# Optimization experiments

Hardware: AMD Instinct MI355X
Metric: run time of the kernel (lower is better)

Reference implementation:

```python
import jax, jax.numpy as jnp
import numpy as np
import math

N, S, D, H, L, F = 4, 2048, 512, 8, 4, 200
HD = D // H
EPS = 1e-5


def _pos_encoding(seq_len, d_model, dtype):
    pos = jnp.arange(seq_len, dtype=jnp.float32)[:, None]            # [S,1]
    div = jnp.exp(jnp.arange(0, d_model, 2, dtype=jnp.float32) * (-math.log(10000.0) / d_model))
    ang = pos * div                                                   # [S,D/2]
    pe = jnp.stack([jnp.sin(ang), jnp.cos(ang)], axis=-1).reshape(seq_len, d_model)
    return pe.astype(dtype)


def _layernorm(x, w, b):
    mu = jnp.mean(x, axis=-1, keepdims=True)
    var = jnp.mean(jnp.square(x - mu), axis=-1, keepdims=True)
    return (x - mu) * jax.lax.rsqrt(var + EPS) * w + b


def setup_inputs() -> dict:
    key = jax.random.key(0)
    ks = jax.random.split(key, 8)
    std = 0.02
    inp = {
        "features": jax.random.normal(ks[0], (N, S, D), dtype=jnp.float32),
        # attention projections, stored as [L, in, out] (math-equivalent to torch x @ W.T + b)
        "Wq": jax.random.normal(ks[1], (L, D, D), dtype=jnp.float32) * std,
        "bq": jnp.zeros((L, D), dtype=jnp.float32),
        "Wk": jax.random.normal(ks[2], (L, D, D), dtype=jnp.float32) * std,
        "bk": jnp.zeros((L, D), dtype=jnp.float32),
        "Wv": jax.random.normal(ks[3], (L, D, D), dtype=jnp.float32) * std,
        "bv": jnp.zeros((L, D), dtype=jnp.float32),
        "Wo": jax.random.normal(ks[4], (L, D, D), dtype=jnp.float32) * std,
        "bo": jnp.zeros((L, D), dtype=jnp.float32),
        # FFN
        "W1": jax.random.normal(ks[5], (L, D, F), dtype=jnp.float32) * std,
        "b1": jnp.zeros((L, F), dtype=jnp.float32),
        "W2": jax.random.normal(ks[6], (L, F, D), dtype=jnp.float32) * std,
        "b2": jnp.zeros((L, D), dtype=jnp.float32),
        # layernorms
        "ln1_w": jnp.ones((L, D), dtype=jnp.float32),
        "ln1_b": jnp.zeros((L, D), dtype=jnp.float32),
        "ln2_w": jnp.ones((L, D), dtype=jnp.float32),
        "ln2_b": jnp.zeros((L, D), dtype=jnp.float32),
    }
    return inp


def _encoder(features, Wq, bq, Wk, bk, Wv, bv, Wo, bo, W1, b1, W2, b2,
             ln1_w, ln1_b, ln2_w, ln2_b):
    n, s, d = features.shape
    x = features + _pos_encoding(s, d, features.dtype)[None]  # PositionalEncoding (dropout=identity in eval)
    scale = 1.0 / math.sqrt(HD)
    for l in range(L):
        # MultiHeadAttention: manual QK^T -> softmax -> AV
        q = (x @ Wq[l] + bq[l]).reshape(n, s, H, HD)
        k = (x @ Wk[l] + bk[l]).reshape(n, s, H, HD)
        v = (x @ Wv[l] + bv[l]).reshape(n, s, H, HD)
        attn = jnp.einsum("nshd,nthd->nhst", q, k) * scale          # [N,H,S,S]
        score = jax.nn.softmax(attn, axis=-1)
        y = jnp.einsum("nhst,nthd->nshd", score, v).reshape(n, s, d)
        attn_out = y @ Wo[l] + bo[l]
        x = _layernorm(x + attn_out, ln1_w[l], ln1_b[l])
        # FFN: linear2(relu(linear1(x)))
        ff = jax.nn.relu(x @ W1[l] + b1[l]) @ W2[l] + b2[l]
        x = _layernorm(x + ff, ln2_w[l], ln2_b[l])
    return x


def reference(features, Wq, bq, Wk, bk, Wv, bv, Wo, bo, W1, b1, W2, b2,
              ln1_w, ln1_b, ln2_w, ln2_b):
    return _encoder(features, Wq, bq, Wk, bk, Wv, bv, Wo, bo, W1, b1, W2, b2,
                    ln1_w, ln1_b, ln2_w, ln2_b)
```

## Files before the change

kernel.cpp:

```cpp
#include <hip/hip_runtime.h>
#include <hip/hip_bf16.h>
#include <cstdint>


typedef __bf16 bf16;
typedef __bf16 bf16x8 __attribute__((ext_vector_type(8)));
typedef __bf16 bf16x4 __attribute__((ext_vector_type(4)));
typedef short short4v __attribute__((ext_vector_type(4)));
typedef float f32x4 __attribute__((ext_vector_type(4)));

#define MFMA16(a, b, c) __builtin_amdgcn_mfma_f32_16x16x32_bf16((a), (b), (c), 0, 0, 0)

__device__ __forceinline__ f32x4 mfma_k16(bf16x4 a, bf16x4 b, f32x4 c) {
#if __has_builtin(__builtin_amdgcn_mfma_f32_16x16x16_bf16)
    return __builtin_amdgcn_mfma_f32_16x16x16_bf16(a, b, c, 0, 0, 0);
#else
    short4v as, bs;
    __builtin_memcpy(&as, &a, 8);
    __builtin_memcpy(&bs, &b, 8);
    return __builtin_amdgcn_mfma_f32_16x16x16bf16_1k(as, bs, c, 0, 0, 0);
#endif
}

static constexpr int NB   = 4;
static constexpr int SQ   = 2048;
static constexpr int DM   = 512;
static constexpr int NH   = 8;
static constexpr int HD   = 64;
static constexpr int NL   = 4;
static constexpr int FF   = 200;
static constexpr int FFP  = 256;
static constexpr int MTOK = NB * SQ;

__device__ __forceinline__ float fast_exp2(float x) {
#if __has_builtin(__builtin_amdgcn_exp2f)
    return __builtin_amdgcn_exp2f(x);
#else
    return exp2f(x);
#endif
}

__device__ __forceinline__ void gld16(bf16* l, const bf16* g) {
    __builtin_amdgcn_global_load_lds(
        (const __attribute__((address_space(1))) void*)g,
        (__attribute__((address_space(3))) void*)l, 16, 0, 0);
}

__global__ __launch_bounds__(256) void convw_kernel(
    const float* __restrict__ Wq, const float* __restrict__ Wk,
    const float* __restrict__ Wv, const float* __restrict__ Wo,
    const float* __restrict__ W1, const float* __restrict__ W2,
    bf16* __restrict__ wqkvt, bf16* __restrict__ wot,
    bf16* __restrict__ w1t, bf16* __restrict__ w2t)
{
    __shared__ float tile[32][33];
    const int z = blockIdx.z, l = z / 6, which = z % 6;
    const float* src; bf16* dst; int K, Nsrc, Npad, Kpad;
    switch (which) {
        case 0: src = Wq + (size_t)l*DM*DM; dst = wqkvt + (size_t)(l*3+0)*DM*DM; K=DM; Nsrc=DM; Npad=DM; Kpad=DM; break;
        case 1: src = Wk + (size_t)l*DM*DM; dst = wqkvt + (size_t)(l*3+1)*DM*DM; K=DM; Nsrc=DM; Npad=DM; Kpad=DM; break;
        case 2: src = Wv + (size_t)l*DM*DM; dst = wqkvt + (size_t)(l*3+2)*DM*DM; K=DM; Nsrc=DM; Npad=DM; Kpad=DM; break;
        case 3: src = Wo + (size_t)l*DM*DM; dst = wot   + (size_t)l*DM*DM;       K=DM; Nsrc=DM; Npad=DM; Kpad=DM; break;
        case 4: src = W1 + (size_t)l*DM*FF; dst = w1t   + (size_t)l*FFP*DM;      K=DM; Nsrc=FF; Npad=FFP; Kpad=DM; break;
        default:src = W2 + (size_t)l*FF*DM; dst = w2t   + (size_t)l*DM*FFP;      K=FF; Nsrc=DM; Npad=DM; Kpad=FFP; break;
    }
    const int k0 = blockIdx.x * 32, n0 = blockIdx.y * 32;
    if (k0 >= Kpad || n0 >= Npad) return;
    const int tr = threadIdx.x >> 3, tc = (threadIdx.x & 7) * 4;
    for (int c = 0; c < 4; c++) {
        int sr = k0 + tr, sc = n0 + tc + c;
        tile[tr][tc + c] = (sr < K && sc < Nsrc) ? src[(size_t)sr * Nsrc + sc] : 0.f;
    }
    __syncthreads();
    const int dr = n0 + tr;
    if (dr < Npad) {
        for (int c = 0; c < 4; c++) {
            int dc = k0 + tc + c;
            if (dc < Kpad) dst[(size_t)dr * Kpad + dc] = (bf16)tile[tc + c][tr];
        }
    }
}

__global__ __launch_bounds__(256) void posenc_kernel(
    const float* __restrict__ f, float* __restrict__ x, bf16* __restrict__ xb)
{
    const int t = blockIdx.x * 256 + threadIdx.x;
    const int d2 = t & 255, row = t >> 8, s = row & (SQ - 1);
    const float kfac = -0.03597789207803197f;
    float dv = __expf((float)d2 * kfac);
    float ang = (float)s * dv;
    float pe0 = sinf(ang), pe1 = cosf(ang);
    const size_t base = (size_t)row * DM + d2 * 2;
    float2 fv = *(const float2*)(f + base);
    float o0 = fv.x + pe0, o1 = fv.y + pe1;
    *(float2*)(x + base) = make_float2(o0, o1);
    union { bf16 h[2]; unsigned int u; } pk;
    pk.h[0] = (bf16)o0; pk.h[1] = (bf16)o1;
    *(unsigned int*)(xb + base) = pk.u;
}

__device__ __forceinline__ void gemm128_core(
    const bf16* __restrict__ A, const bf16* __restrict__ Wt, int K,
    int m0, int n0, bf16* As, bf16* Bs, f32x4 (&acc)[4][4])
{
    const int tid = threadIdx.x;
    const int w = tid >> 6, lane = tid & 63;
    const int l15 = lane & 15, quad = lane >> 4;
    const int srow = w * 16 + (lane >> 2);
    const int scol = (lane & 3) * 8;
    const bf16* Ag = A  + (size_t)(m0 + srow) * K + scol;
    const bf16* Bg = Wt + (size_t)(n0 + srow) * K + scol;
    bf16* AsW = As + w * 512;
    bf16* BsW = Bs + w * 512;
    const int wm = (w >> 1) * 64, wn = (w & 1) * 64;

    for (int k0 = 0; k0 < K; k0 += 32) {
        __syncthreads();
        gld16(AsW,        Ag + k0);
        gld16(AsW + 2048, Ag + (size_t)64 * K + k0);
        gld16(BsW,        Bg + k0);
        gld16(BsW + 2048, Bg + (size_t)64 * K + k0);
        asm volatile("s_waitcnt vmcnt(0)" ::: "memory");
        __syncthreads();

        bf16x8 af[4], bfr[4];
        #pragma unroll
        for (int i = 0; i < 4; i++)
            af[i] = *(const bf16x8*)&As[(wm + i * 16 + l15) * 32 + quad * 8];
        #pragma unroll
        for (int j = 0; j < 4; j++)
            bfr[j] = *(const bf16x8*)&Bs[(wn + j * 16 + l15) * 32 + quad * 8];
        #pragma unroll
        for (int i = 0; i < 4; i++)
            #pragma unroll
            for (int j = 0; j < 4; j++)
                acc[i][j] = MFMA16(af[i], bfr[j], acc[i][j]);
    }
}

__global__ __launch_bounds__(256, 3) void gemm128_kernel(
    const bf16* __restrict__ A, const bf16* __restrict__ Wt,
    const float* __restrict__ bias, int nbias,
    float* __restrict__ outf, bf16* __restrict__ outb,
    int K, int Nc, int mode)
{
    __shared__ alignas(16) bf16 As[128 * 32];
    __shared__ alignas(16) bf16 Bs[128 * 32];
    const int m0 = blockIdx.x * 128, n0 = blockIdx.y * 128;
    f32x4 acc[4][4] = {};
    gemm128_core(A, Wt, K, m0, n0, As, Bs, acc);

    const int lane = threadIdx.x & 63;
    const int l15 = lane & 15, quad = lane >> 4;
    const int w = threadIdx.x >> 6;
    const int wm = (w >> 1) * 64, wn = (w & 1) * 64;
    #pragma unroll
    for (int j = 0; j < 4; j++) {
        const int col = n0 + wn + j * 16 + l15;
        const float bv = (col < nbias) ? bias[col] : 0.f;
        #pragma unroll
        for (int i = 0; i < 4; i++) {
            const int rbase = m0 + wm + i * 16 + quad * 4;
            #pragma unroll
            for (int r = 0; r < 4; r++) {
                float v = acc[i][j][r] + bv;
                const int row = rbase + r;
                const size_t idx = (size_t)row * Nc + col;
                if (mode == 0)      outf[idx] = v;
                else if (mode == 1) outb[idx] = (bf16)v;
                else                outb[idx] = (bf16)fmaxf(v, 0.f);
            }
        }
    }
}

__global__ __launch_bounds__(256, 3) void gemm128_qkv_kernel(
    const bf16* __restrict__ xb, const bf16* __restrict__ Wt,
    const float* __restrict__ bq, const float* __restrict__ bk,
    const float* __restrict__ bv,
    bf16* __restrict__ qb, bf16* __restrict__ kb, bf16* __restrict__ vtb)
{
    __shared__ alignas(16) bf16 As[128 * 32];
    __shared__ alignas(16) bf16 Bs[128 * 32];
    const int m0 = blockIdx.x * 128, n0 = blockIdx.y * 128;
    f32x4 acc[4][4] = {};
    gemm128_core(xb, Wt, DM, m0, n0, As, Bs, acc);

    const int lane = threadIdx.x & 63;
    const int l15 = lane & 15, quad = lane >> 4;
    const int w = threadIdx.x >> 6;
    const int wm = (w >> 1) * 64, wn = (w & 1) * 64;
    const int which = n0 >> 9;
    const float* bias = (which == 0) ? bq : (which == 1) ? bk : bv;
    const float scale = (which == 0) ? 0.18033688f : 1.f;
    #pragma unroll
    for (int j = 0; j < 4; j++) {
        const int c = (n0 & 511) + wn + j * 16 + l15;
        const float bvv = bias[c];
        #pragma unroll
        for (int i = 0; i < 4; i++) {
            const int rbase = m0 + wm + i * 16 + quad * 4;
            #pragma unroll
            for (int r = 0; r < 4; r++) {
                float v = (acc[i][j][r] + bvv) * scale;
                const int row = rbase + r;
                if (which == 0)      qb[(size_t)row * DM + c] = (bf16)v;
                else if (which == 1) kb[(size_t)row * DM + c] = (bf16)v;
                else {
                    const int n = row >> 11, s = row & (SQ - 1);
                    const int h = c >> 6, hd = c & 63;
                    vtb[((size_t)(((n << 3) | h) << 6 | hd) << 11) | s] = (bf16)v;
                }
            }
        }
    }
}

__global__ __launch_bounds__(256, 2) void attn_kernel(
    const bf16* __restrict__ qb, const bf16* __restrict__ kb,
    const bf16* __restrict__ vtb,
    bf16* __restrict__ opart0, bf16* __restrict__ opart1,
    float* __restrict__ lpart)
{
    __shared__ alignas(16) bf16 Kt[2][64][72];
    __shared__ alignas(16) bf16 Vt[2 * 64 * 68];
    const int tid = threadIdx.x;
    const int w = tid >> 6, lane = tid & 63;
    const int l15 = lane & 15, quad = lane >> 4;
    const int id = blockIdx.x;
    const int kvhalf = id & 1;
    const int nh = (id >> 1) & 31;
    const int qblk = id >> 6;
    const int n = nh >> 3, h = nh & 7;
    const int q0 = qblk * 128 + w * 32;
    const int kvbase = kvhalf * (SQ / 2);
    const bf16* qbase = qb + (size_t)n * SQ * DM + h * HD;
    const bf16* kbase = kb + (size_t)n * SQ * DM + h * HD;
    const bf16* vbase = vtb + (size_t)nh * HD * SQ;

    bf16x8 qf[2][2];
    for (int mi = 0; mi < 2; mi++)
        for (int hh = 0; hh < 2; hh++)
            qf[mi][hh] = *(const bf16x8*)(qbase + (size_t)(q0 + mi*16 + l15) * DM + hh*32 + quad*8);

    f32x4 o[2][4] = {};
    float lsum[2] = {0.f, 0.f};

    const int srow = tid >> 2, seg = (tid & 3) * 16;
    const bf16* krow = kbase + (size_t)(kvbase + srow) * DM + seg;
    const bf16* vrow = vbase + (size_t)srow * SQ + kvbase + seg;

    auto storeV = [&](int buf, bf16x8 a, bf16x8 b) {
        bf16* d = &Vt[(buf * 64 + srow) * 68 + seg];
        bf16x4 p0, p1, p2, p3;
        #pragma unroll
        for (int i = 0; i < 4; i++) { p0[i]=a[i]; p1[i]=a[i+4]; p2[i]=b[i]; p3[i]=b[i+4]; }
        *(bf16x4*)(d)      = p0;
        *(bf16x4*)(d + 4)  = p1;
        *(bf16x4*)(d + 8)  = p2;
        *(bf16x4*)(d + 12) = p3;
    };

    {
        bf16x8 k0 = *(const bf16x8*)(krow);
        bf16x8 k1 = *(const bf16x8*)(krow + 8);
        bf16x8 v0 = *(const bf16x8*)(vrow);
        bf16x8 v1 = *(const bf16x8*)(vrow + 8);
        *(bf16x8*)&Kt[0][srow][seg]     = k0;
        *(bf16x8*)&Kt[0][srow][seg + 8] = k1;
        storeV(0, v0, v1);
    }

    const int NT = SQ / 128;
    for (int jt = 0; jt < NT; jt++) {
        const int buf = jt & 1;
        __syncthreads();
        const bool pre = (jt + 1 < NT);
        bf16x8 k0, k1, v0, v1;
        if (pre) {
            const bf16* kp = krow + (size_t)(jt + 1) * 64 * DM;
            const bf16* vp = vrow + (jt + 1) * 64;
            k0 = *(const bf16x8*)(kp);
            k1 = *(const bf16x8*)(kp + 8);
            v0 = *(const bf16x8*)(vp);
            v1 = *(const bf16x8*)(vp + 8);
        }

        #pragma unroll
        for (int s4 = 0; s4 < 4; s4++) {
            bf16x8 kf0 = *(const bf16x8*)&Kt[buf][s4*16 + l15][quad*8];
            bf16x8 kf1 = *(const bf16x8*)&Kt[buf][s4*16 + l15][32 + quad*8];
            bf16x4 pf[2];
            #pragma unroll
            for (int mi = 0; mi < 2; mi++) {
                f32x4 sacc = {};
                sacc = MFMA16(kf0, qf[mi][0], sacc);
                sacc = MFMA16(kf1, qf[mi][1], sacc);
                float p0 = fast_exp2(sacc[0]);
                float p1 = fast_exp2(sacc[1]);
                float p2 = fast_exp2(sacc[2]);
                float p3 = fast_exp2(sacc[3]);
                lsum[mi] += (p0 + p1) + (p2 + p3);
                bf16x4 pk;
                pk[0] = (bf16)p0; pk[1] = (bf16)p1;
                pk[2] = (bf16)p2; pk[3] = (bf16)p3;
                pf[mi] = pk;
            }
            #pragma unroll
            for (int d4 = 0; d4 < 4; d4++) {
                bf16x4 vf = *(const bf16x4*)&Vt[(buf*64 + d4*16 + l15) * 68 + s4*16 + quad*4];
                o[0][d4] = mfma_k16(pf[0], vf, o[0][d4]);
                o[1][d4] = mfma_k16(pf[1], vf, o[1][d4]);
            }
        }

        if (pre) {
            *(bf16x8*)&Kt[buf^1][srow][seg]     = k0;
            *(bf16x8*)&Kt[buf^1][srow][seg + 8] = k1;
            storeV(buf^1, v0, v1);
        }
    }

    #pragma unroll
    for (int mi = 0; mi < 2; mi++) {
        lsum[mi] += __shfl_xor(lsum[mi], 16, 64);
        lsum[mi] += __shfl_xor(lsum[mi], 32, 64);
    }
    if (lane < 16) {
        const int qg = (nh << 11) + q0 + lane;
        lpart[(kvhalf << 16) + qg]      = lsum[0];
        lpart[(kvhalf << 16) + qg + 16] = lsum[1];
    }

    bf16* op = kvhalf ? opart1 : opart0;
    #pragma unroll
    for (int mi = 0; mi < 2; mi++) {
        #pragma unroll
        for (int d4 = 0; d4 < 4; d4++) {
            const int col = h * HD + d4 * 16 + l15;
            #pragma unroll
            for (int r = 0; r < 4; r++) {
                const int row = n * SQ + q0 + mi*16 + quad*4 + r;
                op[(size_t)row * DM + col] = (bf16)o[mi][d4][r];
            }
        }
    }
}

__global__ __launch_bounds__(256) void attn_combine_kernel(
    const bf16* o0, const bf16* o1, const float* __restrict__ lpart,
    bf16* yb)
{
    const int w = threadIdx.x >> 6, lane = threadIdx.x & 63;
    const size_t row = (size_t)blockIdx.x * 4 + w;
    const int q = (int)(row & (SQ - 1));
    const int nh = (int)(row >> 11) * 8 + (lane >> 3);
    const float rl = 1.f / (lpart[(nh << 11) + q] + lpart[(1 << 16) + (nh << 11) + q]);
    const size_t base = row * DM + lane * 8;
    bf16x8 a = *(const bf16x8*)(o0 + base);
    bf16x8 b = *(const bf16x8*)(o1 + base);
    bf16x8 y;
    #pragma unroll
    for (int i = 0; i < 8; i++)
        y[i] = (bf16)(((float)a[i] + (float)b[i]) * rl);
    *(bf16x8*)(yb + base) = y;
}

__global__ __launch_bounds__(256) void ln_kernel(
    const float* __restrict__ res, const float* __restrict__ add,
    const float* __restrict__ g, const float* __restrict__ beta,
    float* __restrict__ outf, bf16* __restrict__ outb)
{
    const int w = threadIdx.x >> 6, lane = threadIdx.x & 63;
    const size_t row = (size_t)blockIdx.x * 4 + w;
    const float4* rp = (const float4*)(res + row * DM);
    const float4* ap = (const float4*)(add + row * DM);
    float4 v[2];
    float s = 0.f, s2 = 0.f;
    #pragma unroll
    for (int i = 0; i < 2; i++) {
        const int idx = i * 64 + lane;
        float4 a = rp[idx], c = ap[idx];
        float x0 = a.x + c.x, x1 = a.y + c.y, x2 = a.z + c.z, x3 = a.w + c.w;
        v[i] = make_float4(x0, x1, x2, x3);
        s  += x0 + x1 + x2 + x3;
        s2 += x0*x0 + x1*x1 + x2*x2 + x3*x3;
    }
    for (int m = 1; m < 64; m <<= 1) {
        s  += __shfl_xor(s,  m, 64);
        s2 += __shfl_xor(s2, m, 64);
    }
    const float mean = s * (1.f / DM);
    const float var  = s2 * (1.f / DM) - mean * mean;
    const float rstd = rsqrtf(var + 1e-5f);
    #pragma unroll
    for (int i = 0; i < 2; i++) {
        const int idx = i * 64 + lane;
        float4 gw = ((const float4*)g)[idx], bw = ((const float4*)beta)[idx];
        float o0 = (v[i].x - mean) * rstd * gw.x + bw.x;
        float o1 = (v[i].y - mean) * rstd * gw.y + bw.y;
        float o2 = (v[i].z - mean) * rstd * gw.z + bw.z;
        float o3 = (v[i].w - mean) * rstd * gw.w + bw.w;
        ((float4*)(outf + row * DM))[idx] = make_float4(o0, o1, o2, o3);
        union { bf16 h[4]; uint2 u; } pk;
        pk.h[0] = (bf16)o0; pk.h[1] = (bf16)o1; pk.h[2] = (bf16)o2; pk.h[3] = (bf16)o3;
        *(uint2*)(outb + row * DM + idx * 4) = pk.u;
    }
}

extern "C" void kernel_launch(void* const* d_in, const int* in_sizes, int n_in,
                              void* d_out, int out_size, void* d_ws, size_t ws_size,
                              hipStream_t stream)
{
    const float* features = (const float*)d_in[0];
    const float* Wq  = (const float*)d_in[1];
    const float* bq  = (const float*)d_in[2];
    const float* Wk  = (const float*)d_in[3];
    const float* bk  = (const float*)d_in[4];
    const float* Wv  = (const float*)d_in[5];
    const float* bv  = (const float*)d_in[6];
    const float* Wo  = (const float*)d_in[7];
    const float* bo  = (const float*)d_in[8];
    const float* W1  = (const float*)d_in[9];
    const float* b1  = (const float*)d_in[10];
    const float* W2  = (const float*)d_in[11];
    const float* b2  = (const float*)d_in[12];
    const float* ln1w = (const float*)d_in[13];
    const float* ln1b = (const float*)d_in[14];
    const float* ln2w = (const float*)d_in[15];
    const float* ln2b = (const float*)d_in[16];
    float* outp = (float*)d_out;

    char* p = (char*)d_ws;
    size_t off = 0;
    auto alloc = [&](size_t bytes) { void* r = p + off; off = (off + bytes + 255) & ~(size_t)255; return r; };
    const size_t tokD = (size_t)MTOK * DM;
    float* x     = (float*)alloc(tokD * 4);
    float* tmp   = (float*)alloc(tokD * 4);
    bf16* xb     = (bf16*)alloc(tokD * 2);
    bf16* qb     = (bf16*)alloc(tokD * 2);
    bf16* kb     = (bf16*)alloc(tokD * 2);
    bf16* vtb    = (bf16*)alloc(tokD * 2);
    bf16* yb     = (bf16*)alloc(tokD * 2);
    bf16* opart1 = (bf16*)alloc(tokD * 2);
    float* lpart = (float*)alloc(2 * 65536 * 4);
    bf16* ffh    = (bf16*)alloc((size_t)MTOK * FFP * 2);
    bf16* wqkvt  = (bf16*)alloc((size_t)NL * 3 * DM * DM * 2);
    bf16* wot    = (bf16*)alloc((size_t)NL * DM * DM * 2);
    bf16* w1t    = (bf16*)alloc((size_t)NL * FFP * DM * 2);
    bf16* w2t    = (bf16*)alloc((size_t)NL * DM * FFP * 2);
    (void)ws_size; (void)in_sizes; (void)n_in; (void)out_size;

    convw_kernel<<<dim3(16, 16, NL * 6), 256, 0, stream>>>(
        Wq, Wk, Wv, Wo, W1, W2, wqkvt, wot, w1t, w2t);

    posenc_kernel<<<MTOK, 256, 0, stream>>>(features, x, xb);

    for (int l = 0; l < NL; l++) {
        const bf16* wqkvt_l = wqkvt + (size_t)l * 3 * DM * DM;
        gemm128_qkv_kernel<<<dim3(MTOK / 128, 1536 / 128), 256, 0, stream>>>(
            xb, wqkvt_l, bq + l*DM, bk + l*DM, bv + l*DM, qb, kb, vtb);
        attn_kernel<<<1024, 256, 0, stream>>>(qb, kb, vtb, yb, opart1, lpart);
        attn_combine_kernel<<<MTOK / 4, 256, 0, stream>>>(yb, opart1, lpart, yb);
        gemm128_kernel<<<dim3(MTOK / 128, DM / 128), 256, 0, stream>>>(
            yb, wot + (size_t)l*DM*DM, bo + l*DM, DM, tmp, nullptr, DM, DM, 0);
        ln_kernel<<<MTOK / 4, 256, 0, stream>>>(x, tmp, ln1w + l*DM, ln1b + l*DM, x, xb);
        gemm128_kernel<<<dim3(MTOK / 128, FFP / 128), 256, 0, stream>>>(
            xb, w1t + (size_t)l*FFP*DM, b1 + l*FF, FF, nullptr, ffh, DM, FFP, 2);
        gemm128_kernel<<<dim3(MTOK / 128, DM / 128), 256, 0, stream>>>(
            ffh, w2t + (size_t)l*DM*FFP, b2 + l*DM, DM, tmp, nullptr, FFP, DM, 0);
        float* outdst = (l == NL - 1) ? outp : x;
        ln_kernel<<<MTOK / 4, 256, 0, stream>>>(x, tmp, ln2w + l*DM, ln2b + l*DM, outdst, xb);
    }
}
```

Before: 681.3 us.

## Use 128x64 GEMM tiles for small GEMMs and 64-query-per-wave attention blocks

Replaces the 128x128 GEMM used for the output projection and the two FFN linears with a new 128x64-tile kernel, doubling the number of workgroups so the small-N GEMMs fill more compute units. The attention kernel now processes 64 queries per wave (four 16-row MFMA tiles) instead of 32, halving the grid and reusing each K/V tile loaded into LDS across twice as many queries. This raises register pressure in the attention kernel (more accumulators and Q fragments) and may lower occupancy, and the GEMM change trades fewer B loads per block for more blocks.

```diff
diff --git a/kernel.cpp b/kernel.cpp
--- a/kernel.cpp
+++ b/kernel.cpp
@@ -138,24 +138,51 @@
     }
 }
 
-__global__ __launch_bounds__(256, 3) void gemm128_kernel(
+__global__ __launch_bounds__(256, 3) void gemm64_kernel(
     const bf16* __restrict__ A, const bf16* __restrict__ Wt,
     const float* __restrict__ bias, int nbias,
     float* __restrict__ outf, bf16* __restrict__ outb,
     int K, int Nc, int mode)
 {
     __shared__ alignas(16) bf16 As[128 * 32];
-    __shared__ alignas(16) bf16 Bs[128 * 32];
-    const int m0 = blockIdx.x * 128, n0 = blockIdx.y * 128;
-    f32x4 acc[4][4] = {};
-    gemm128_core(A, Wt, K, m0, n0, As, Bs, acc);
-
-    const int lane = threadIdx.x & 63;
+    __shared__ alignas(16) bf16 Bs[64 * 32];
+    const int m0 = blockIdx.x * 128, n0 = blockIdx.y * 64;
+    const int tid = threadIdx.x;
+    const int w = tid >> 6, lane = tid & 63;
     const int l15 = lane & 15, quad = lane >> 4;
-    const int w = threadIdx.x >> 6;
-    const int wm = (w >> 1) * 64, wn = (w & 1) * 64;
-    #pragma unroll
-    for (int j = 0; j < 4; j++) {
+    const int srow = w * 16 + (lane >> 2);
+    const int scol = (lane & 3) * 8;
+    const bf16* Ag = A  + (size_t)(m0 + srow) * K + scol;
+    const bf16* Bg = Wt + (size_t)(n0 + srow) * K + scol;
+    bf16* AsW = As + w * 512;
+    bf16* BsW = Bs + w * 512;
+    const int wm = (w >> 1) * 64, wn = (w & 1) * 32;
+    f32x4 acc[4][2] = {};
+
+    for (int k0 = 0; k0 < K; k0 += 32) {
+        __syncthreads();
+        gld16(AsW,        Ag + k0);
+        gld16(AsW + 2048, Ag + (size_t)64 * K + k0);
+        gld16(BsW,        Bg + k0);
+        asm volatile("s_waitcnt vmcnt(0)" ::: "memory");
+        __syncthreads();
+
+        bf16x8 af[4], bfr[2];
+        #pragma unroll
+        for (int i = 0; i < 4; i++)
+            af[i] = *(const bf16x8*)&As[(wm + i * 16 + l15) * 32 + quad * 8];
+        #pragma unroll
+        for (int j = 0; j < 2; j++)
+            bfr[j] = *(const bf16x8*)&Bs[(wn + j * 16 + l15) * 32 + quad * 8];
+        #pragma unroll
+        for (int i = 0; i < 4; i++)
+            #pragma unroll
+            for (int j = 0; j < 2; j++)
+                acc[i][j] = MFMA16(af[i], bfr[j], acc[i][j]);
+    }
+
+    #pragma unroll
+    for (int j = 0; j < 2; j++) {
         const int col = n0 + wn + j * 16 + l15;
         const float bv = (col < nbias) ? bias[col] : 0.f;
         #pragma unroll
@@ -232,19 +259,21 @@
     const int nh = (id >> 1) & 31;
     const int qblk = id >> 6;
     const int n = nh >> 3, h = nh & 7;
-    const int q0 = qblk * 128 + w * 32;
+    const int q0 = qblk * 256 + w * 64;
     const int kvbase = kvhalf * (SQ / 2);
     const bf16* qbase = qb + (size_t)n * SQ * DM + h * HD;
     const bf16* kbase = kb + (size_t)n * SQ * DM + h * HD;
     const bf16* vbase = vtb + (size_t)nh * HD * SQ;
 
-    bf16x8 qf[2][2];
-    for (int mi = 0; mi < 2; mi++)
+    bf16x8 qf[4][2];
+    #pragma unroll
+    for (int mi = 0; mi < 4; mi++)
+        #pragma unroll
         for (int hh = 0; hh < 2; hh++)
             qf[mi][hh] = *(const bf16x8*)(qbase + (size_t)(q0 + mi*16 + l15) * DM + hh*32 + quad*8);
 
-    f32x4 o[2][4] = {};
-    float lsum[2] = {0.f, 0.f};
+    f32x4 o[4][4] = {};
+    float lsum[4] = {0.f, 0.f, 0.f, 0.f};
 
     const int srow = tid >> 2, seg = (tid & 3) * 16;
     const bf16* krow = kbase + (size_t)(kvbase + srow) * DM + seg;
@@ -290,9 +319,9 @@
         for (int s4 = 0; s4 < 4; s4++) {
             bf16x8 kf0 = *(const bf16x8*)&Kt[buf][s4*16 + l15][quad*8];
             bf16x8 kf1 = *(const bf16x8*)&Kt[buf][s4*16 + l15][32 + quad*8];
-            bf16x4 pf[2];
-            #pragma unroll
-            for (int mi = 0; mi < 2; mi++) {
+            bf16x4 pf[4];
+            #pragma unroll
+            for (int mi = 0; mi < 4; mi++) {
                 f32x4 sacc = {};
                 sacc = MFMA16(kf0, qf[mi][0], sacc);
                 sacc = MFMA16(kf1, qf[mi][1], sacc);
@@ -309,8 +338,9 @@
             #pragma unroll
             for (int d4 = 0; d4 < 4; d4++) {
                 bf16x4 vf = *(const bf16x4*)&Vt[(buf*64 + d4*16 + l15) * 68 + s4*16 + quad*4];
-                o[0][d4] = mfma_k16(pf[0], vf, o[0][d4]);
-                o[1][d4] = mfma_k16(pf[1], vf, o[1][d4]);
+                #pragma unroll
+                for (int mi = 0; mi < 4; mi++)
+                    o[mi][d4] = mfma_k16(pf[mi], vf, o[mi][d4]);
             }
         }
 
@@ -322,19 +352,20 @@
     }
 
     #pragma unroll
-    for (int mi = 0; mi < 2; mi++) {
+    for (int mi = 0; mi < 4; mi++) {
         lsum[mi] += __shfl_xor(lsum[mi], 16, 64);
         lsum[mi] += __shfl_xor(lsum[mi], 32, 64);
     }
     if (lane < 16) {
         const int qg = (nh << 11) + q0 + lane;
-        lpart[(kvhalf << 16) + qg]      = lsum[0];
-        lpart[(kvhalf << 16) + qg + 16] = lsum[1];
+        #pragma unroll
+        for (int mi = 0; mi < 4; mi++)
+            lpart[(kvhalf << 16) + qg + mi * 16] = lsum[mi];
     }
 
     bf16* op = kvhalf ? opart1 : opart0;
     #pragma unroll
-    for (int mi = 0; mi < 2; mi++) {
+    for (int mi = 0; mi < 4; mi++) {
         #pragma unroll
         for (int d4 = 0; d4 < 4; d4++) {
             const int col = h * HD + d4 * 16 + l15;
@@ -460,14 +491,14 @@
         const bf16* wqkvt_l = wqkvt + (size_t)l * 3 * DM * DM;
         gemm128_qkv_kernel<<<dim3(MTOK / 128, 1536 / 128), 256, 0, stream>>>(
             xb, wqkvt_l, bq + l*DM, bk + l*DM, bv + l*DM, qb, kb, vtb);
-        attn_kernel<<<1024, 256, 0, stream>>>(qb, kb, vtb, yb, opart1, lpart);
+        attn_kernel<<<512, 256, 0, stream>>>(qb, kb, vtb, yb, opart1, lpart);
         attn_combine_kernel<<<MTOK / 4, 256, 0, stream>>>(yb, opart1, lpart, yb);
-        gemm128_kernel<<<dim3(MTOK / 128, DM / 128), 256, 0, stream>>>(
+        gemm64_kernel<<<dim3(MTOK / 128, DM / 64), 256, 0, stream>>>(
             yb, wot + (size_t)l*DM*DM, bo + l*DM, DM, tmp, nullptr, DM, DM, 0);
         ln_kernel<<<MTOK / 4, 256, 0, stream>>>(x, tmp, ln1w + l*DM, ln1b + l*DM, x, xb);
-        gemm128_kernel<<<dim3(MTOK / 128, FFP / 128), 256, 0, stream>>>(
+        gemm64_kernel<<<dim3(MTOK / 128, FFP / 64), 256, 0, stream>>>(
             xb, w1t + (size_t)l*FFP*DM, b1 + l*FF, FF, nullptr, ffh, DM, FFP, 2);
-        gemm128_kernel<<<dim3(MTOK / 128, DM / 128), 256, 0, stream>>>(
+        gemm64_kernel<<<dim3(MTOK / 128, DM / 64), 256, 0, stream>>>(
             ffh, w2t + (size_t)l*DM*FFP, b2 + l*DM, DM, tmp, nullptr, FFP, DM, 0);
         float* outdst = (l == NL - 1) ? outp : x;
         ln_kernel<<<MTOK / 4, 256, 0, stream>>>(x, tmp, ln2w + l*DM, ln2b + l*DM, outdst, xb);
```

Measured after the change: 642.4 us. 5.7% less time.
